# Optimization experiments

Measured on AMD Instinct MI355X. Metric: run time of the kernel, lower is better.

The kernel has to match this reference:

```python
import jax, jax.numpy as jnp
import numpy as np

B = 65536       # batch of (head, tail) triples
S = 512         # num_neg_samples
D = 100         # embed_size
HV = 100000     # head entity vocab
TV = 188047     # tail entity vocab (hard-coded 188047 in original)


def setup_inputs() -> dict:
    key = jax.random.key(0)
    k1, k2, k3, k4, k5, k6 = jax.random.split(key, 6)
    initrange = 0.5 / D
    head_table = jax.random.uniform(k1, (HV + 1, D), minval=-initrange, maxval=initrange, dtype=jnp.float32)
    tail_table = jax.random.uniform(k2, (TV + 1, D), minval=-initrange, maxval=initrange, dtype=jnp.float32)
    rel_vec = jax.random.uniform(k3, (1, D), minval=-initrange, maxval=initrange, dtype=jnp.float32)
    rel_bias = jnp.zeros((TV + 1,), dtype=jnp.float32)  # original inits bias to zeros
    head_idx = jax.random.randint(k4, (B,), 0, HV)
    tail_idx = jax.random.randint(k5, (B,), 0, TV)
    # stands in for torch.multinomial(distrib, num_samples, replacement=True)
    neg_idx = jax.random.randint(k6, (S,), 0, TV)
    return dict(head_table=head_table, tail_table=tail_table, rel_vec=rel_vec,
                rel_bias=rel_bias, head_idx=head_idx, tail_idx=tail_idx, neg_idx=neg_idx)


def reference(head_table, tail_table, rel_vec, rel_bias, head_idx, tail_idx, neg_idx):
    # entity_head_vec = entity_head_embed(idxs); example_vec = head + relation
    h = head_table[head_idx]                      # [B, D]
    ex = h + rel_vec                              # [B, D]
    t = tail_table[tail_idx]                      # [B, D]
    bias = rel_bias[tail_idx]                     # [B]
    # pos_logits = bmm(pos_vec, example_vec) + relation_bias
    pos_logits = jnp.einsum('bd,bd->b', t, ex) + bias
    pos_loss = -jax.nn.log_sigmoid(pos_logits)    # = -log(sigmoid(x)), stable
    # shared negatives: neg_logits = example_vec @ neg_vec.T + bias
    neg = tail_table[neg_idx]                     # [S, D]
    neg_logits = ex @ neg.T + bias[:, None]       # [B, S]
    neg_loss = -jax.nn.log_sigmoid(-neg_logits).sum(axis=1)
    return jnp.mean(pos_loss + neg_loss)
```

## Files before the change

### kernel.cpp

```cpp
#include <hip/hip_runtime.h>
#include <stdint.h>

typedef __attribute__((ext_vector_type(4))) float   f4;
typedef __attribute__((ext_vector_type(8))) short   short8;
typedef __attribute__((ext_vector_type(4))) float   floatx4;
typedef __attribute__((ext_vector_type(4))) unsigned int u32x4;

#define LN2F 0.6931471805599453f

#define BB 65536
#define SS 512
#define DD 100

__device__ __forceinline__ unsigned short f2bf(float f) {
  union { float f; unsigned int u; } v; v.f = f;
  unsigned int u = v.u;
  u += 0x7fffu + ((u >> 16) & 1u);
  return (unsigned short)(u >> 16);
}
__device__ __forceinline__ float bf2f(short s) {
  union { float f; unsigned int u; } v;
  v.u = ((unsigned int)(unsigned short)s) << 16;
  return v.f;
}
__device__ __forceinline__ u32x4 pack8(f4 a, f4 b) {
  u32x4 r;
  r.x = (unsigned int)f2bf(a[0]) | ((unsigned int)f2bf(a[1]) << 16);
  r.y = (unsigned int)f2bf(a[2]) | ((unsigned int)f2bf(a[3]) << 16);
  r.z = (unsigned int)f2bf(b[0]) | ((unsigned int)f2bf(b[1]) << 16);
  r.w = (unsigned int)f2bf(b[2]) | ((unsigned int)f2bf(b[3]) << 16);
  return r;
}
__device__ __forceinline__ float softplus_full(float x) {
  return fmaxf(x, 0.f) + log1pf(expf(-fabsf(x)));
}

__global__ __launch_bounds__(256) void negprep_k(
    const float* __restrict__ tail_table, const int* __restrict__ neg_idx,
    u32x4* __restrict__ nws, float* __restrict__ out) {
  if (blockIdx.x == 0 && threadIdx.x == 0) out[0] = 0.f;
  int tid = blockIdx.x * 256 + threadIdx.x;
  int s = tid >> 4, kg = tid & 15, k0 = kg * 8;
  int nrow = neg_idx[s];
  const float* np = tail_table + (size_t)nrow * DD;
  f4 a = {0.f,0.f,0.f,0.f}, b = {0.f,0.f,0.f,0.f};
  if (kg < 12)       { a = *(const f4*)(np + k0); b = *(const f4*)(np + k0 + 4); }
  else if (kg == 12) { a = *(const f4*)(np + 96); }
  nws[((s >> 4) * 4 + (kg >> 2)) * 64 + (s & 15) + 16 * (kg & 3)] = pack8(a, b);
}

__device__ __forceinline__ float neg_pass_fast(
    const short8* __restrict__ exAs, const short8* __restrict__ nfr,
    const float* __restrict__ bias_s, int w, int lane, int quad, float& amax) {
  float sx = 0.f, sxx = 0.f;
  amax = 0.f;
  #pragma unroll
  for (int h = 0; h < 2; ++h) {
    short8 afr[2][4];
    float  br[2][4];
    #pragma unroll
    for (int m = 0; m < 2; ++m) {
      int mf = h * 2 + m;
      #pragma unroll
      for (int ks = 0; ks < 4; ++ks) afr[m][ks] = exAs[(mf * 4 + ks) * 64 + lane];
      #pragma unroll
      for (int r = 0; r < 4; ++r)   br[m][r]  = bias_s[mf * 16 + quad * 4 + r];
    }
    #pragma unroll 2
    for (int g = 0; g < 8; ++g) {
      int ng = w * 8 + g;
      short8 bfr[4];
      #pragma unroll
      for (int ks = 0; ks < 4; ++ks)
        bfr[ks] = nfr[(ng * 4 + ks) * 64 + lane];
      floatx4 acc[2];
      #pragma unroll
      for (int m = 0; m < 2; ++m) {
        floatx4 c; c[0] = br[m][0]; c[1] = br[m][1]; c[2] = br[m][2]; c[3] = br[m][3];
        acc[m] = c;
      }
      #pragma unroll
      for (int ks = 0; ks < 4; ++ks)
        #pragma unroll
        for (int m = 0; m < 2; ++m)
          acc[m] = __builtin_amdgcn_mfma_f32_16x16x32_bf16(afr[m][ks], bfr[ks], acc[m], 0, 0, 0);
      #pragma unroll
      for (int m = 0; m < 2; ++m)
        #pragma unroll
        for (int r = 0; r < 4; ++r) {
          float x = acc[m][r];
          sx += x;
          sxx = fmaf(x, x, sxx);
          amax = fmaxf(amax, fabsf(x));
        }
    }
  }
  return fmaf(sx, 0.5f, fmaf(sxx, 0.125f, 128.f * LN2F));
}

__device__ __attribute__((noinline)) float neg_pass_full(
    const short8* __restrict__ exAs, const short8* __restrict__ nfr,
    const float* __restrict__ bias_s, int w, int lane, int quad) {
  float nacc = 0.f;
  for (int h = 0; h < 2; ++h) {
    short8 afr[2][4];
    float  br[2][4];
    for (int m = 0; m < 2; ++m) {
      int mf = h * 2 + m;
      for (int ks = 0; ks < 4; ++ks) afr[m][ks] = exAs[(mf * 4 + ks) * 64 + lane];
      for (int r = 0; r < 4; ++r)   br[m][r]  = bias_s[mf * 16 + quad * 4 + r];
    }
    for (int g = 0; g < 8; ++g) {
      int ng = w * 8 + g;
      short8 bfr[4];
      for (int ks = 0; ks < 4; ++ks) bfr[ks] = nfr[(ng * 4 + ks) * 64 + lane];
      floatx4 acc[2];
      for (int m = 0; m < 2; ++m) {
        floatx4 c; c[0] = br[m][0]; c[1] = br[m][1]; c[2] = br[m][2]; c[3] = br[m][3];
        acc[m] = c;
      }
      for (int ks = 0; ks < 4; ++ks)
        for (int m = 0; m < 2; ++m)
          acc[m] = __builtin_amdgcn_mfma_f32_16x16x32_bf16(afr[m][ks], bfr[ks], acc[m], 0, 0, 0);
      for (int m = 0; m < 2; ++m)
        for (int r = 0; r < 4; ++r)
          nacc += softplus_full(acc[m][r]);
    }
  }
  return nacc;
}

__global__ __launch_bounds__(256, 4) void keg_main(
    const float* __restrict__ head_table, const float* __restrict__ tail_table,
    const float* __restrict__ rel_vec,   const float* __restrict__ rel_bias,
    const int* __restrict__ head_idx,    const int* __restrict__ tail_idx,
    const u32x4* __restrict__ nws,       float* __restrict__ out) {
  __shared__ u32x4 exA4[1024];
  __shared__ float bias_s[64];
  __shared__ float red[4];

  const int t = threadIdx.x;
  const int kg = t & 15, k0 = kg * 8, rid = t >> 4;
  const int bbase = blockIdx.x * 64;

  #pragma unroll
  for (int p = 0; p < 4; ++p) {
    int r  = p * 16 + rid;
    int gb = bbase + r;
    int hrow = head_idx[gb];
    const float* hp = head_table + (size_t)hrow * DD;
    f4 a = {0,0,0,0}, b = {0,0,0,0}, ra = {0,0,0,0}, rb = {0,0,0,0};
    if (kg < 12) {
      a  = *(const f4*)(hp + k0);       b  = *(const f4*)(hp + k0 + 4);
      ra = *(const f4*)(rel_vec + k0);  rb = *(const f4*)(rel_vec + k0 + 4);
    } else if (kg == 12) {
      a  = *(const f4*)(hp + 96);       ra = *(const f4*)(rel_vec + 96);
    }
    f4 e0 = a + ra, e1 = b + rb;
    exA4[(p * 4 + (kg >> 2)) * 64 + rid + 16 * (kg & 3)] = pack8(e0, e1);
    if (kg == 0) bias_s[r] = rel_bias[tail_idx[gb]];
  }
  __syncthreads();

  const int w = t >> 6, lane = t & 63;
  const int m15 = lane & 15, quad = lane >> 4;
  const short8* exAs = (const short8*)exA4;

  float pos_acc = 0.f;
  {
    int rloc = w * 16 + m15;
    int gb = bbase + rloc;
    int trow = tail_idx[gb];
    const float* tp = tail_table + (size_t)trow * DD;
    float pdot = 0.f;
    #pragma unroll
    for (int ks = 0; ks < 4; ++ks) {
      short8 ev = exAs[(w * 4 + ks) * 64 + lane];
      int kk = ks * 32 + quad * 8;
      f4 ta = {0,0,0,0}, tb = {0,0,0,0};
      if (kk < 96)       { ta = *(const f4*)(tp + kk); tb = *(const f4*)(tp + kk + 4); }
      else if (kk == 96) { ta = *(const f4*)(tp + 96); }
      pdot += bf2f(ev[0])*ta[0] + bf2f(ev[1])*ta[1] + bf2f(ev[2])*ta[2] + bf2f(ev[3])*ta[3];
      pdot += bf2f(ev[4])*tb[0] + bf2f(ev[5])*tb[1] + bf2f(ev[6])*tb[2] + bf2f(ev[7])*tb[3];
    }
    pdot += __shfl_xor(pdot, 16);
    pdot += __shfl_xor(pdot, 32);
    if (lane < 16) {
      float logit = pdot + bias_s[rloc];
      pos_acc = softplus_full(-logit);
    }
  }

  const short8* nfr = (const short8*)nws;
  float amax;
  float nacc = neg_pass_fast(exAs, nfr, bias_s, w, lane, quad, amax);
  if (__ballot(amax < 0.03f) != ~0ULL)
    nacc = neg_pass_full(exAs, nfr, bias_s, w, lane, quad);

  float tot = nacc + pos_acc;
  #pragma unroll
  for (int off = 32; off; off >>= 1) tot += __shfl_down(tot, off);
  if (lane == 0) red[w] = tot;
  __syncthreads();
  if (t == 0)
    atomicAdd(out, (red[0] + red[1] + red[2] + red[3]) * (1.0f / (float)BB));
}

extern "C" void kernel_launch(void* const* d_in, const int* in_sizes, int n_in,
                              void* d_out, int out_size, void* d_ws, size_t ws_size,
                              hipStream_t stream) {
  const float* head_table = (const float*)d_in[0];
  const float* tail_table = (const float*)d_in[1];
  const float* rel_vec    = (const float*)d_in[2];
  const float* rel_bias   = (const float*)d_in[3];
  const int*   head_idx   = (const int*)d_in[4];
  const int*   tail_idx   = (const int*)d_in[5];
  const int*   neg_idx    = (const int*)d_in[6];
  float* out = (float*)d_out;

  u32x4* nws = (u32x4*)d_ws;

  negprep_k<<<32, 256, 0, stream>>>(tail_table, neg_idx, nws, out);
  keg_main<<<1024, 256, 0, stream>>>(head_table, tail_table, rel_vec, rel_bias,
                                     head_idx, tail_idx, (const u32x4*)nws, out);
}
```

Before: 162.2 us.

## Fuse positive dot into gather stage and fall back to full softplus per tile

Each thread now loads its head and tail row chunks together up front, computes the positive-pair dot product in fp32 during the gather and reduces it with lane shuffles. This replaces the separate pass that re-read the bf16 example tile from shared memory and fetched tail rows again. Row loads are made unconditional, with masking afterwards, so the gathers are issued without branches. The noinline whole-block recompute used when the Taylor approximation is unsafe is replaced by a per-tile ballot that chooses exact softplus or the series. This avoids redoing all the MFMA work, at the cost of a ballot per tile and some extra over-read of adjacent memory.

```diff
diff --git a/kernel.cpp b/kernel.cpp
--- a/kernel.cpp
+++ b/kernel.cpp
@@ -17,11 +17,6 @@
   unsigned int u = v.u;
   u += 0x7fffu + ((u >> 16) & 1u);
   return (unsigned short)(u >> 16);
-}
-__device__ __forceinline__ float bf2f(short s) {
-  union { float f; unsigned int u; } v;
-  v.u = ((unsigned int)(unsigned short)s) << 16;
-  return v.f;
 }
 __device__ __forceinline__ u32x4 pack8(f4 a, f4 b) {
   u32x4 r;
@@ -43,17 +38,71 @@
   int s = tid >> 4, kg = tid & 15, k0 = kg * 8;
   int nrow = neg_idx[s];
   const float* np = tail_table + (size_t)nrow * DD;
-  f4 a = {0.f,0.f,0.f,0.f}, b = {0.f,0.f,0.f,0.f};
-  if (kg < 12)       { a = *(const f4*)(np + k0); b = *(const f4*)(np + k0 + 4); }
-  else if (kg == 12) { a = *(const f4*)(np + 96); }
+  f4 a = *(const f4*)(np + k0);
+  f4 b = *(const f4*)(np + k0 + 4);
+  if (kg > 12)  a = (f4){0.f,0.f,0.f,0.f};
+  if (kg >= 12) b = (f4){0.f,0.f,0.f,0.f};
   nws[((s >> 4) * 4 + (kg >> 2)) * 64 + (s & 15) + 16 * (kg & 3)] = pack8(a, b);
 }
 
-__device__ __forceinline__ float neg_pass_fast(
-    const short8* __restrict__ exAs, const short8* __restrict__ nfr,
-    const float* __restrict__ bias_s, int w, int lane, int quad, float& amax) {
-  float sx = 0.f, sxx = 0.f;
-  amax = 0.f;
+__global__ __launch_bounds__(256, 4) void keg_main(
+    const float* __restrict__ head_table, const float* __restrict__ tail_table,
+    const float* __restrict__ rel_vec,   const float* __restrict__ rel_bias,
+    const int* __restrict__ head_idx,    const int* __restrict__ tail_idx,
+    const u32x4* __restrict__ nws,       float* __restrict__ out) {
+  __shared__ u32x4 exA4[1024];
+  __shared__ float bias_s[64];
+  __shared__ float red[4];
+
+  const int t = threadIdx.x;
+  const int kg = t & 15, rid = t >> 4, k0 = kg * 8;
+  const int bbase = blockIdx.x * 64;
+
+  f4 ra = {0,0,0,0}, rb = {0,0,0,0};
+  if (kg <= 12) ra = *(const f4*)(rel_vec + k0);
+  if (kg <  12) rb = *(const f4*)(rel_vec + k0 + 4);
+
+  const float* hp[4]; const float* tp[4];
+  float biasv[4];
+  #pragma unroll
+  for (int p = 0; p < 4; ++p) {
+    int R = bbase + p * 16 + rid;
+    hp[p] = head_table + (size_t)head_idx[R] * DD;
+    int trow = tail_idx[R];
+    tp[p] = tail_table + (size_t)trow * DD;
+    biasv[p] = rel_bias[trow];
+  }
+  f4 ha[4], hb[4], ta[4], tb[4];
+  #pragma unroll
+  for (int p = 0; p < 4; ++p) {
+    ha[p] = *(const f4*)(hp[p] + k0);
+    hb[p] = *(const f4*)(hp[p] + k0 + 4);
+    ta[p] = *(const f4*)(tp[p] + k0);
+    tb[p] = *(const f4*)(tp[p] + k0 + 4);
+  }
+
+  float pos_acc = 0.f;
+  #pragma unroll
+  for (int p = 0; p < 4; ++p) {
+    f4 e0 = ha[p] + ra, e1 = hb[p] + rb;
+    if (kg > 12)  e0 = (f4){0.f,0.f,0.f,0.f};
+    if (kg >= 12) e1 = (f4){0.f,0.f,0.f,0.f};
+    exA4[(p * 4 + (kg >> 2)) * 64 + rid + 16 * (kg & 3)] = pack8(e0, e1);
+    float d = e0[0]*ta[p][0] + e0[1]*ta[p][1] + e0[2]*ta[p][2] + e0[3]*ta[p][3]
+            + e1[0]*tb[p][0] + e1[1]*tb[p][1] + e1[2]*tb[p][2] + e1[3]*tb[p][3];
+    d += __shfl_xor(d, 1); d += __shfl_xor(d, 2);
+    d += __shfl_xor(d, 4); d += __shfl_xor(d, 8);
+    if (kg == 0) {
+      bias_s[p * 16 + rid] = biasv[p];
+      pos_acc += softplus_full(-(d + biasv[p]));
+    }
+  }
+  __syncthreads();
+
+  const int w = t >> 6, lane = t & 63, quad = lane >> 4;
+  const short8* exAs = (const short8*)exA4;
+  const short8* nf   = (const short8*)nws;
+  float nacc = 0.f;
   #pragma unroll
   for (int h = 0; h < 2; ++h) {
     short8 afr[2][4];
@@ -72,11 +121,11 @@
       short8 bfr[4];
       #pragma unroll
       for (int ks = 0; ks < 4; ++ks)
-        bfr[ks] = nfr[(ng * 4 + ks) * 64 + lane];
+        bfr[ks] = nf[(ng * 4 + ks) * 64 + lane];
       floatx4 acc[2];
       #pragma unroll
       for (int m = 0; m < 2; ++m) {
-        floatx4 c; c[0] = br[m][0]; c[1] = br[m][1]; c[2] = br[m][2]; c[3] = br[m][3];
+        floatx4 c; c[0]=br[m][0]; c[1]=br[m][1]; c[2]=br[m][2]; c[3]=br[m][3];
         acc[m] = c;
       }
       #pragma unroll
@@ -84,118 +133,27 @@
         #pragma unroll
         for (int m = 0; m < 2; ++m)
           acc[m] = __builtin_amdgcn_mfma_f32_16x16x32_bf16(afr[m][ks], bfr[ks], acc[m], 0, 0, 0);
+      float s1 = 0.f, s2 = 0.f, gmax = 0.f;
       #pragma unroll
       for (int m = 0; m < 2; ++m)
         #pragma unroll
         for (int r = 0; r < 4; ++r) {
           float x = acc[m][r];
-          sx += x;
-          sxx = fmaf(x, x, sxx);
-          amax = fmaxf(amax, fabsf(x));
+          s1 += x;
+          s2 = fmaf(x, x, s2);
+          gmax = fmaxf(gmax, fabsf(x));
         }
+      if (__ballot(gmax < 0.03f) == ~0ULL) {
+        nacc += fmaf(s1, 0.5f, fmaf(s2, 0.125f, 8.f * LN2F));
+      } else {
+        #pragma unroll
+        for (int m = 0; m < 2; ++m)
+          #pragma unroll
+          for (int r = 0; r < 4; ++r)
+            nacc += softplus_full(acc[m][r]);
+      }
     }
   }
-  return fmaf(sx, 0.5f, fmaf(sxx, 0.125f, 128.f * LN2F));
-}
-
-__device__ __attribute__((noinline)) float neg_pass_full(
-    const short8* __restrict__ exAs, const short8* __restrict__ nfr,
-    const float* __restrict__ bias_s, int w, int lane, int quad) {
-  float nacc = 0.f;
-  for (int h = 0; h < 2; ++h) {
-    short8 afr[2][4];
-    float  br[2][4];
-    for (int m = 0; m < 2; ++m) {
-      int mf = h * 2 + m;
-      for (int ks = 0; ks < 4; ++ks) afr[m][ks] = exAs[(mf * 4 + ks) * 64 + lane];
-      for (int r = 0; r < 4; ++r)   br[m][r]  = bias_s[mf * 16 + quad * 4 + r];
-    }
-    for (int g = 0; g < 8; ++g) {
-      int ng = w * 8 + g;
-      short8 bfr[4];
-      for (int ks = 0; ks < 4; ++ks) bfr[ks] = nfr[(ng * 4 + ks) * 64 + lane];
-      floatx4 acc[2];
-      for (int m = 0; m < 2; ++m) {
-        floatx4 c; c[0] = br[m][0]; c[1] = br[m][1]; c[2] = br[m][2]; c[3] = br[m][3];
-        acc[m] = c;
-      }
-      for (int ks = 0; ks < 4; ++ks)
-        for (int m = 0; m < 2; ++m)
-          acc[m] = __builtin_amdgcn_mfma_f32_16x16x32_bf16(afr[m][ks], bfr[ks], acc[m], 0, 0, 0);
-      for (int m = 0; m < 2; ++m)
-        for (int r = 0; r < 4; ++r)
-          nacc += softplus_full(acc[m][r]);
-    }
-  }
-  return nacc;
-}
-
-__global__ __launch_bounds__(256, 4) void keg_main(
-    const float* __restrict__ head_table, const float* __restrict__ tail_table,
-    const float* __restrict__ rel_vec,   const float* __restrict__ rel_bias,
-    const int* __restrict__ head_idx,    const int* __restrict__ tail_idx,
-    const u32x4* __restrict__ nws,       float* __restrict__ out) {
-  __shared__ u32x4 exA4[1024];
-  __shared__ float bias_s[64];
-  __shared__ float red[4];
-
-  const int t = threadIdx.x;
-  const int kg = t & 15, k0 = kg * 8, rid = t >> 4;
-  const int bbase = blockIdx.x * 64;
-
-  #pragma unroll
-  for (int p = 0; p < 4; ++p) {
-    int r  = p * 16 + rid;
-    int gb = bbase + r;
-    int hrow = head_idx[gb];
-    const float* hp = head_table + (size_t)hrow * DD;
-    f4 a = {0,0,0,0}, b = {0,0,0,0}, ra = {0,0,0,0}, rb = {0,0,0,0};
-    if (kg < 12) {
-      a  = *(const f4*)(hp + k0);       b  = *(const f4*)(hp + k0 + 4);
-      ra = *(const f4*)(rel_vec + k0);  rb = *(const f4*)(rel_vec + k0 + 4);
-    } else if (kg == 12) {
-      a  = *(const f4*)(hp + 96);       ra = *(const f4*)(rel_vec + 96);
-    }
-    f4 e0 = a + ra, e1 = b + rb;
-    exA4[(p * 4 + (kg >> 2)) * 64 + rid + 16 * (kg & 3)] = pack8(e0, e1);
-    if (kg == 0) bias_s[r] = rel_bias[tail_idx[gb]];
-  }
-  __syncthreads();
-
-  const int w = t >> 6, lane = t & 63;
-  const int m15 = lane & 15, quad = lane >> 4;
-  const short8* exAs = (const short8*)exA4;
-
-  float pos_acc = 0.f;
-  {
-    int rloc = w * 16 + m15;
-    int gb = bbase + rloc;
-    int trow = tail_idx[gb];
-    const float* tp = tail_table + (size_t)trow * DD;
-    float pdot = 0.f;
-    #pragma unroll
-    for (int ks = 0; ks < 4; ++ks) {
-      short8 ev = exAs[(w * 4 + ks) * 64 + lane];
-      int kk = ks * 32 + quad * 8;
-      f4 ta = {0,0,0,0}, tb = {0,0,0,0};
-      if (kk < 96)       { ta = *(const f4*)(tp + kk); tb = *(const f4*)(tp + kk + 4); }
-      else if (kk == 96) { ta = *(const f4*)(tp + 96); }
-      pdot += bf2f(ev[0])*ta[0] + bf2f(ev[1])*ta[1] + bf2f(ev[2])*ta[2] + bf2f(ev[3])*ta[3];
-      pdot += bf2f(ev[4])*tb[0] + bf2f(ev[5])*tb[1] + bf2f(ev[6])*tb[2] + bf2f(ev[7])*tb[3];
-    }
-    pdot += __shfl_xor(pdot, 16);
-    pdot += __shfl_xor(pdot, 32);
-    if (lane < 16) {
-      float logit = pdot + bias_s[rloc];
-      pos_acc = softplus_full(-logit);
-    }
-  }
-
-  const short8* nfr = (const short8*)nws;
-  float amax;
-  float nacc = neg_pass_fast(exAs, nfr, bias_s, w, lane, quad, amax);
-  if (__ballot(amax < 0.03f) != ~0ULL)
-    nacc = neg_pass_full(exAs, nfr, bias_s, w, lane, quad);
 
   float tot = nacc + pos_acc;
   #pragma unroll
```

After: 160.1 us. No clear change (-1.2%).
